# Kernel optimization log

Measured on AMD Instinct MI355X. Metric: run time of the kernel, lower is better.

The kernel has to match this reference:

```python
import jax, jax.numpy as jnp
import numpy as np

# Dimensions: B jets, P max particles, C coords, F features, K neighbors,
# H hidden units, O MLP output dim. Edge feature dim E = 2*(C+F).
B, P, C, F, K, H, O = 256, 128, 2, 7, 16, 128, 256
E = 2 * (C + F)
BIG = 1e9  # distance assigned to invalid (padded) neighbors


def setup_inputs() -> dict:
    key = jax.random.key(0)
    k1, k2, k3, k4 = jax.random.split(key, 4)
    raw = jax.random.normal(k1, (B, P, C + F), dtype=jnp.float32)
    # per-jet particle counts in [K+2, P]; padding is contiguous at the end
    lengths = jax.random.randint(k2, (B,), K + 2, P + 1)
    mask = (jnp.arange(P)[None, :] < lengths[:, None]).astype(jnp.float32)  # [B,P]
    # zero out padded rows and append mask as the last column (as the layer expects)
    x = jnp.concatenate([raw * mask[..., None], mask[..., None]], axis=-1)  # [B,P,C+F+1]
    W1 = jax.random.normal(k3, (E, H), dtype=jnp.float32) * (1.0 / np.sqrt(E))
    b1 = jnp.zeros((H,), dtype=jnp.float32)
    W2 = jax.random.normal(k4, (H, O), dtype=jnp.float32) * (1.0 / np.sqrt(H))
    b2 = jnp.zeros((O,), dtype=jnp.float32)
    return {"x": x, "W1": W1, "b1": b1, "W2": W2, "b2": b2}


def reference(x, W1, b1, W2, b2):
    coords = x[..., :C]          # [B,P,C]
    feats = x[..., C:-1]         # [B,P,F]
    mask = x[..., -1]            # [B,P] 1=real particle, 0=padding
    valid = mask > 0

    # --- kNN on coordinates (masked, vectorized over jets) ---
    diff = coords[:, :, None, :] - coords[:, None, :, :]      # [B,P,P,C]
    # squared distance: same ordering as tf.norm, avoids sqrt-at-zero issues
    dist2 = jnp.sum(diff * diff, axis=-1)                      # [B,P,P]
    dist2 = jnp.where(valid[:, None, :], dist2, BIG)           # mask padded neighbors
    _, idx = jax.lax.top_k(-dist2, K + 1)                      # [B,P,K+1]
    idx = idx[..., 1:]                                         # drop self -> [B,P,K]

    # --- gather neighbor coords/features ---
    idx_flat = idx.reshape(B, P * K)
    nbr_c = jnp.take_along_axis(coords, idx_flat[..., None], axis=1).reshape(B, P, K, C)
    nbr_f = jnp.take_along_axis(feats, idx_flat[..., None], axis=1).reshape(B, P, K, F)
    ctr_c = jnp.broadcast_to(coords[:, :, None, :], (B, P, K, C))
    ctr_f = jnp.broadcast_to(feats[:, :, None, :], (B, P, K, F))

    # edge features: [coord_i, feat_i, coord_j - coord_i, feat_j - feat_i]
    edge = jnp.concatenate([ctr_c, ctr_f, nbr_c - ctr_c, nbr_f - ctr_f], axis=-1)  # [B,P,K,E]

    # --- MLP + mean aggregation over neighbors ---
    h = jax.nn.relu(edge @ W1 + b1)   # [B,P,K,H]
    h = jax.nn.relu(h @ W2 + b2)      # [B,P,K,O]
    avg = jnp.mean(h, axis=2)         # [B,P,O]

    # append mask column; zero out padded particles (matches _fix_number_of_particles)
    out = jnp.concatenate([avg, jnp.ones((B, P, 1), avg.dtype)], axis=-1) * mask[..., None]
    return out
```

## Files before the change

kernel.cpp:

```cpp
#include <hip/hip_runtime.h>

#define BB 256
#define PP 128
#define KK 16
#define HH 128
#define OO 256
#define EE 18
#define XCH 10
#define BIGD 1000000000.0f
#define GPT 16
#define PH 8
#define NBLK ((BB * PP) / GPT)

typedef __bf16 bf16x8 __attribute__((ext_vector_type(8)));
typedef __bf16 bf16x4 __attribute__((ext_vector_type(4)));
typedef float  f32x4  __attribute__((ext_vector_type(4)));

__global__ __launch_bounds__(256) void pack_w_kernel(const float* __restrict__ W1,
                                                     const float* __restrict__ W2,
                                                     __bf16* __restrict__ W2p,
                                                     __bf16* __restrict__ W1p) {
    const int t = blockIdx.x * 256 + threadIdx.x;
    if (t < 32768) {
        const int j  = t & 7;
        const int l  = (t >> 3) & 63;
        const int ks = (t >> 9) & 3;
        const int ct = t >> 11;
        const int row = ks * 32 + ((l >> 4) * 8) + j;
        const int col = ct * 16 + (l & 15);
        W2p[t] = (__bf16)W2[row * OO + col];
    } else {
        const int t2 = t - 32768;
        const int j  = t2 & 7;
        const int l  = (t2 >> 3) & 63;
        const int nt = t2 >> 9;
        const int k  = ((l >> 4) * 8) + j;
        const int n  = nt * 16 + (l & 15);
        W1p[t2] = (k < EE) ? (__bf16)W1[k * HH + n] : (__bf16)0.0f;
    }
}

__global__ __launch_bounds__(256, 4) void mlp_kernel(const float* __restrict__ x,
                                                     const __bf16* __restrict__ W1p,
                                                     const float* __restrict__ b1,
                                                     const __bf16* __restrict__ W2p,
                                                     const float* __restrict__ b2,
                                                     float* __restrict__ out) {
    __shared__ __bf16 sh1A[4 * PH * 64 * 8];
    __shared__ int    sknn[PH][KK];

    const int tid = threadIdx.x;
    const int lane = tid & 63;
    const int w = tid >> 6;
    const int quad = lane >> 4;
    const int lcol = lane & 15;

    const int pbase = blockIdx.x * GPT;
    const int bidx = pbase >> 7;
    const int i0 = pbase & (PP - 1);
    const float* xb = x + (size_t)bidx * PP * XCH;
    float* outrow = out + (size_t)pbase * (OO + 1);

    bf16x8 wf[8];
#pragma unroll
    for (int nt = 0; nt < 8; ++nt)
        wf[nt] = *(const bf16x8*)&W1p[(size_t)((nt * 64 + lane) * 8)];

    const f32x4 z4 = {0.0f, 0.0f, 0.0f, 0.0f};

#pragma unroll
    for (int h = 0; h < 2; ++h) {
        const int r0 = h * PH;

        const float mph = xb[(i0 + r0 + (lane & 7)) * XCH + (XCH - 1)];
        if (__all(mph == 0.0f)) {
            for (int o = tid; o < PH * (OO + 1); o += 256)
                outrow[(size_t)r0 * (OO + 1) + o] = 0.0f;
            continue;
        }

        const int j0 = lane, j1 = lane + 64;
        const float2 c0 = *(const float2*)(xb + j0 * XCH);
        const float  m0 = xb[j0 * XCH + (XCH - 1)];
        const float2 c1 = *(const float2*)(xb + j1 * XCH);
        const float  m1 = xb[j1 * XCH + (XCH - 1)];

#pragma unroll 1
        for (int p = 0; p < 2; ++p) {
            const int g = w * 2 + p;
            const int ip = i0 + r0 + g;
            const float2 cc = *(const float2*)(xb + ip * XCH);
            const float mwp = xb[ip * XCH + (XCH - 1)];
            if (mwp != 0.0f) {
                float d0, d1;
                {
                    float dx = cc.x - c0.x, dy = cc.y - c0.y;
                    d0 = __fadd_rn(__fmul_rn(dx, dx), __fmul_rn(dy, dy));
                    if (m0 <= 0.0f || j0 == ip) d0 = BIGD;
                }
                {
                    float dx = cc.x - c1.x, dy = cc.y - c1.y;
                    d1 = __fadd_rn(__fmul_rn(dx, dx), __fmul_rn(dy, dy));
                    if (m1 <= 0.0f || j1 == ip) d1 = BIGD;
                }

                const unsigned d0b = __float_as_uint(d0);
                const unsigned d1b = __float_as_uint(d1);

                unsigned long long A0 = ~0ull, A1 = ~0ull, W0 = 0ull, W1 = 0ull;
                int need = KK;
                int asz = 2 * 64;

                auto step = [&](unsigned long long q0, unsigned long long q1) {
                    const unsigned long long z0 = A0 & q0;
                    const unsigned long long z1 = A1 & q1;
                    const int c = __popcll(z0) + __popcll(z1);
                    if (c == need) { W0 |= z0; W1 |= z1; A0 = A1 = 0ull; need = 0; }
                    else if (c > need) { A0 = z0; A1 = z1; asz = c; }
                    else { W0 |= z0; W1 |= z1; need -= c; A0 &= ~z0; A1 &= ~z1; asz -= c; }
                };

#pragma unroll 1
                for (int t = 14; t >= 0; --t) {
                    const unsigned dg0 = (d0b >> (2 * t + 1)) & 3u;
                    const unsigned dg1 = (d1b >> (2 * t + 1)) & 3u;
                    const unsigned long long p0_0  = __ballot(dg0 == 0u);
                    const unsigned long long p1_0  = __ballot(dg1 == 0u);
                    const unsigned long long p0_01 = __ballot(dg0 <= 1u);
                    const unsigned long long p1_01 = __ballot(dg1 <= 1u);
                    const unsigned long long p0_02 = __ballot(dg0 <= 2u);
                    const unsigned long long p1_02 = __ballot(dg1 <= 2u);
                    const unsigned long long z0_0  = A0 & p0_0,  z1_0  = A1 & p1_0;
                    const unsigned long long z0_01 = A0 & p0_01, z1_01 = A1 & p1_01;
                    const unsigned long long z0_02 = A0 & p0_02, z1_02 = A1 & p1_02;
                    const int c0c  = __popcll(z0_0)  + __popcll(z1_0);
                    const int c01 = __popcll(z0_01) + __popcll(z1_01);
                    const int c02 = __popcll(z0_02) + __popcll(z1_02);
                    if (c0c >= need) {
                        A0 = z0_0; A1 = z1_0; asz = c0c;
                    } else if (c01 >= need) {
                        W0 |= z0_0; W1 |= z1_0; need -= c0c;
                        A0 = z0_01 & ~p0_0; A1 = z1_01 & ~p1_0; asz = c01 - c0c;
                    } else if (c02 >= need) {
                        W0 |= z0_01; W1 |= z1_01; need -= c01;
                        A0 = z0_02 & ~p0_01; A1 = z1_02 & ~p1_01; asz = c02 - c01;
                    } else {
                        W0 |= z0_02; W1 |= z1_02; need -= c02;
                        A0 &= ~p0_02; A1 &= ~p1_02; asz -= c02;
                    }
                    if (asz == need) { W0 |= A0; W1 |= A1; A0 = A1 = 0ull; need = 0; break; }
                }
                if (need) {
                    const unsigned long long q0 = __ballot((d0b & 1u) == 0u);
                    const unsigned long long q1 = __ballot((d1b & 1u) == 0u);
                    step(q0, q1);
                }
                if (need) step(~0ull, 0ull);
                {
                    const unsigned long long M5 = 0x00000000FFFFFFFFull;
                    const unsigned long long M4 = 0x0000FFFF0000FFFFull;
                    const unsigned long long M3 = 0x00FF00FF00FF00FFull;
                    const unsigned long long M2 = 0x0F0F0F0F0F0F0F0Full;
                    const unsigned long long M1 = 0x3333333333333333ull;
                    const unsigned long long M0 = 0x5555555555555555ull;
                    if (need) step(M5, M5);
                    if (need) step(M4, M4);
                    if (need) step(M3, M3);
                    if (need) step(M2, M2);
                    if (need) step(M1, M1);
                    if (need) step(M0, M0);
                }
                W0 |= A0; W1 |= A1;

                unsigned int mb0 = __builtin_amdgcn_mbcnt_lo((unsigned)(W0 & 0xffffffffull), 0u);
                mb0 = __builtin_amdgcn_mbcnt_hi((unsigned)(W0 >> 32), mb0);
                unsigned int mb1 = __builtin_amdgcn_mbcnt_lo((unsigned)(W1 & 0xffffffffull), 0u);
                mb1 = __builtin_amdgcn_mbcnt_hi((unsigned)(W1 >> 32), mb1);
                const int base1 = __popcll(W0);

                if ((W0 >> lane) & 1ull) sknn[g][mb0] = j0;
                if ((W1 >> lane) & 1ull) sknn[g][base1 + mb1] = j1;
            } else {
                if (lane < KK) sknn[g][lane] = 0;
            }
        }

#pragma unroll
        for (int p = 0; p < 2; ++p) {
            const int g = w * 2 + p;
            const int ip = i0 + r0 + g;
            const int jn = sknn[g][lcol];
            const float* ciP = xb + ip * XCH;
            const float* cjP = xb + jn * XCH;
            const float2 a01 = *(const float2*)(ciP + 0);
            const float2 a23 = *(const float2*)(ciP + 2);
            const float2 a45 = *(const float2*)(ciP + 4);
            const float2 a67 = *(const float2*)(ciP + 6);
            const float  a8  = ciP[8];
            const float2 n01 = *(const float2*)(cjP + 0);
            const float2 n23 = *(const float2*)(cjP + 2);
            const float2 n45 = *(const float2*)(cjP + 4);
            const float2 n67 = *(const float2*)(cjP + 6);
            const float  n8  = cjP[8];

            float v[8];
#pragma unroll
            for (int e = 0; e < 8; ++e) v[e] = 0.0f;
            if (quad == 0) {
                v[0] = a01.x; v[1] = a01.y; v[2] = a23.x; v[3] = a23.y;
                v[4] = a45.x; v[5] = a45.y; v[6] = a67.x; v[7] = a67.y;
            } else if (quad == 1) {
                v[0] = a8;
                v[1] = n01.x - a01.x; v[2] = n01.y - a01.y;
                v[3] = n23.x - a23.x; v[4] = n23.y - a23.y;
                v[5] = n45.x - a45.x; v[6] = n45.y - a45.y;
                v[7] = n67.x - a67.x;
            } else if (quad == 2) {
                v[0] = n67.y - a67.y;
                v[1] = n8 - a8;
            }

            bf16x8 ef;
#pragma unroll
            for (int e = 0; e < 8; ++e) ef[e] = (__bf16)v[e];

            f32x4 hh[8];
#pragma unroll
            for (int nt = 0; nt < 8; ++nt)
                hh[nt] = __builtin_amdgcn_mfma_f32_16x16x32_bf16(wf[nt], ef, z4, 0, 0, 0);

#pragma unroll
            for (int nt = 0; nt < 8; ++nt) {
                const int ks = nt >> 1;
                const int lp = (((nt * 2 + (quad >> 1)) & 3) << 4) | lcol;
                const f32x4 b1v = *(const f32x4*)&b1[nt * 16 + quad * 4];
                bf16x4 hv;
#pragma unroll
                for (int r = 0; r < 4; ++r)
                    hv[r] = (__bf16)fmaxf(hh[nt][r] + b1v[r], 0.0f);
                *(bf16x4*)&sh1A[((ks * PH + g) * 64 + lp) * 8 + (quad & 1) * 4] = hv;
            }
        }
        __syncthreads();

#pragma unroll
        for (int gg = 0; gg < 2; ++gg) {
#pragma unroll
            for (int ch = 0; ch < 2; ++ch) {
                f32x4 acc[4][2];
#pragma unroll
                for (int gi = 0; gi < 4; ++gi) { acc[gi][0] = z4; acc[gi][1] = z4; }

#pragma unroll
                for (int ks = 0; ks < 4; ++ks) {
                    bf16x8 af[4], bfr[2];
#pragma unroll
                    for (int gi = 0; gi < 4; ++gi)
                        af[gi] = *(const bf16x8*)&sh1A[((ks * PH + gg * 4 + gi) * 64 + lane) * 8];
#pragma unroll
                    for (int c = 0; c < 2; ++c)
                        bfr[c] = *(const bf16x8*)&W2p[(size_t)((((w * 4 + ch * 2 + c) * 4 + ks) * 64 + lane) * 8)];
#pragma unroll
                    for (int gi = 0; gi < 4; ++gi)
#pragma unroll
                        for (int c = 0; c < 2; ++c)
                            acc[gi][c] = __builtin_amdgcn_mfma_f32_16x16x32_bf16(
                                af[gi], bfr[c], acc[gi][c], 0, 0, 0);
                }

#pragma unroll
                for (int c = 0; c < 2; ++c) {
                    const int col = w * 64 + (ch * 2 + c) * 16 + lcol;
                    const float bc = b2[col];
                    float val = 0.0f;
#pragma unroll
                    for (int gi = 0; gi < 4; ++gi) {
                        float s = 0.0f;
#pragma unroll
                        for (int r = 0; r < 4; ++r) s += fmaxf(acc[gi][c][r] + bc, 0.0f);
                        s += __shfl_xor(s, 16, 64);
                        s += __shfl_xor(s, 32, 64);
                        if (quad == gi) val = s;
                    }
                    const float mp = xb[(i0 + r0 + gg * 4 + quad) * XCH + (XCH - 1)];
                    outrow[(size_t)(r0 + gg * 4 + quad) * (OO + 1) + col] = val * (mp * (1.0f / KK));
                }
            }
        }
        if (tid < PH)
            outrow[(size_t)(r0 + tid) * (OO + 1) + OO] = xb[(i0 + r0 + tid) * XCH + (XCH - 1)];

        __syncthreads();
    }
}

extern "C" void kernel_launch(void* const* d_in, const int* in_sizes, int n_in,
                              void* d_out, int out_size, void* d_ws, size_t ws_size,
                              hipStream_t stream) {
    const float* x  = (const float*)d_in[0];
    const float* W1 = (const float*)d_in[1];
    const float* b1 = (const float*)d_in[2];
    const float* W2 = (const float*)d_in[3];
    const float* b2 = (const float*)d_in[4];
    float* out = (float*)d_out;

    __bf16* W2p = (__bf16*)d_ws;
    __bf16* W1p = (__bf16*)((char*)d_ws + 65536);

    pack_w_kernel<<<144, 256, 0, stream>>>(W1, W2, W2p, W1p);

    mlp_kernel<<<NBLK, 256, 0, stream>>>(x, W1p, b1, W2p, b2, out);
}
```

Measured before the change: 133.1 us.

## Halve particles per block and interleave two radix-select kNN searches per wave

Each block now handles 8 particles instead of two sequential halves of 8, which doubles the grid and removes the inner half-loop and its extra barrier. Within each wave, the two particles' radix-select kNN loops are interleaved in one loop over digits, so their ballots and popcounts can overlap instead of running back to back. This adds latency hiding and more blocks for the scheduler. The cost is W1 fragment loads and x staging repeated per smaller block, plus extra registers for the two selection states.

```diff
diff --git a/kernel.cpp b/kernel.cpp
--- a/kernel.cpp
+++ b/kernel.cpp
@@ -8,13 +8,13 @@
 #define EE 18
 #define XCH 10
 #define BIGD 1000000000.0f
-#define GPT 16
-#define PH 8
+#define GPT 8
 #define NBLK ((BB * PP) / GPT)
 
 typedef __bf16 bf16x8 __attribute__((ext_vector_type(8)));
 typedef __bf16 bf16x4 __attribute__((ext_vector_type(4)));
 typedef float  f32x4  __attribute__((ext_vector_type(4)));
+typedef unsigned long long ull;
 
 __global__ __launch_bounds__(256) void pack_w_kernel(const float* __restrict__ W1,
                                                      const float* __restrict__ W2,
@@ -46,8 +46,8 @@
                                                      const __bf16* __restrict__ W2p,
                                                      const float* __restrict__ b2,
                                                      float* __restrict__ out) {
-    __shared__ __bf16 sh1A[4 * PH * 64 * 8];
-    __shared__ int    sknn[PH][KK];
+    __shared__ __bf16 sh1A[4 * GPT * 64 * 8];
+    __shared__ int    sknn[GPT][KK];
 
     const int tid = threadIdx.x;
     const int lane = tid & 63;
@@ -61,237 +61,251 @@
     const float* xb = x + (size_t)bidx * PP * XCH;
     float* outrow = out + (size_t)pbase * (OO + 1);
 
+    const float mph = xb[(i0 + (lane & 7)) * XCH + (XCH - 1)];
+    if (__all(mph == 0.0f)) {
+        for (int o = tid; o < GPT * (OO + 1); o += 256) outrow[o] = 0.0f;
+        return;
+    }
+
+    const int j0 = lane, j1 = lane + 64;
+    const float2 c0 = *(const float2*)(xb + j0 * XCH);
+    const float  m0 = xb[j0 * XCH + (XCH - 1)];
+    const float2 c1 = *(const float2*)(xb + j1 * XCH);
+    const float  m1 = xb[j1 * XCH + (XCH - 1)];
+
+    const int gA = w * 2, gB = w * 2 + 1;
+    const int iA = i0 + gA, iB = i0 + gB;
+    const float2 ccA = *(const float2*)(xb + iA * XCH);
+    const float  mA  = xb[iA * XCH + (XCH - 1)];
+    const float2 ccB = *(const float2*)(xb + iB * XCH);
+    const float  mB  = xb[iB * XCH + (XCH - 1)];
+
     bf16x8 wf[8];
 #pragma unroll
     for (int nt = 0; nt < 8; ++nt)
         wf[nt] = *(const bf16x8*)&W1p[(size_t)((nt * 64 + lane) * 8)];
 
-    const f32x4 z4 = {0.0f, 0.0f, 0.0f, 0.0f};
-
-#pragma unroll
-    for (int h = 0; h < 2; ++h) {
-        const int r0 = h * PH;
-
-        const float mph = xb[(i0 + r0 + (lane & 7)) * XCH + (XCH - 1)];
-        if (__all(mph == 0.0f)) {
-            for (int o = tid; o < PH * (OO + 1); o += 256)
-                outrow[(size_t)r0 * (OO + 1) + o] = 0.0f;
-            continue;
-        }
-
-        const int j0 = lane, j1 = lane + 64;
-        const float2 c0 = *(const float2*)(xb + j0 * XCH);
-        const float  m0 = xb[j0 * XCH + (XCH - 1)];
-        const float2 c1 = *(const float2*)(xb + j1 * XCH);
-        const float  m1 = xb[j1 * XCH + (XCH - 1)];
+    unsigned db0[2], db1[2];
+    {
+        float dx, dy, d;
+        dx = ccA.x - c0.x; dy = ccA.y - c0.y;
+        d = __fadd_rn(__fmul_rn(dx, dx), __fmul_rn(dy, dy));
+        if (m0 <= 0.0f || j0 == iA) d = BIGD;
+        db0[0] = __float_as_uint(d);
+        dx = ccA.x - c1.x; dy = ccA.y - c1.y;
+        d = __fadd_rn(__fmul_rn(dx, dx), __fmul_rn(dy, dy));
+        if (m1 <= 0.0f || j1 == iA) d = BIGD;
+        db1[0] = __float_as_uint(d);
+        dx = ccB.x - c0.x; dy = ccB.y - c0.y;
+        d = __fadd_rn(__fmul_rn(dx, dx), __fmul_rn(dy, dy));
+        if (m0 <= 0.0f || j0 == iB) d = BIGD;
+        db0[1] = __float_as_uint(d);
+        dx = ccB.x - c1.x; dy = ccB.y - c1.y;
+        d = __fadd_rn(__fmul_rn(dx, dx), __fmul_rn(dy, dy));
+        if (m1 <= 0.0f || j1 == iB) d = BIGD;
+        db1[1] = __float_as_uint(d);
+    }
+
+    const bool act[2] = {mA != 0.0f, mB != 0.0f};
+    ull A0[2], A1[2], W0[2], W1g[2];
+    int need[2], asz[2];
+#pragma unroll
+    for (int p = 0; p < 2; ++p) {
+        A0[p] = ~0ull; A1[p] = ~0ull; W0[p] = 0ull; W1g[p] = 0ull;
+        need[p] = act[p] ? KK : 0;
+        asz[p] = 128;
+    }
 
 #pragma unroll 1
+    for (int t = 14; t >= 0; --t) {
+#pragma unroll
         for (int p = 0; p < 2; ++p) {
-            const int g = w * 2 + p;
-            const int ip = i0 + r0 + g;
-            const float2 cc = *(const float2*)(xb + ip * XCH);
-            const float mwp = xb[ip * XCH + (XCH - 1)];
-            if (mwp != 0.0f) {
-                float d0, d1;
-                {
-                    float dx = cc.x - c0.x, dy = cc.y - c0.y;
-                    d0 = __fadd_rn(__fmul_rn(dx, dx), __fmul_rn(dy, dy));
-                    if (m0 <= 0.0f || j0 == ip) d0 = BIGD;
+            if (need[p]) {
+                const unsigned dg0 = (db0[p] >> (2 * t + 1)) & 3u;
+                const unsigned dg1 = (db1[p] >> (2 * t + 1)) & 3u;
+                const ull p0_0  = __ballot(dg0 == 0u);
+                const ull p1_0  = __ballot(dg1 == 0u);
+                const ull p0_01 = __ballot(dg0 <= 1u);
+                const ull p1_01 = __ballot(dg1 <= 1u);
+                const ull p0_02 = __ballot(dg0 <= 2u);
+                const ull p1_02 = __ballot(dg1 <= 2u);
+                const ull z0_0  = A0[p] & p0_0,  z1_0  = A1[p] & p1_0;
+                const ull z0_01 = A0[p] & p0_01, z1_01 = A1[p] & p1_01;
+                const ull z0_02 = A0[p] & p0_02, z1_02 = A1[p] & p1_02;
+                const int c0c = __popcll(z0_0)  + __popcll(z1_0);
+                const int c01 = __popcll(z0_01) + __popcll(z1_01);
+                const int c02 = __popcll(z0_02) + __popcll(z1_02);
+                if (c0c >= need[p]) {
+                    A0[p] = z0_0; A1[p] = z1_0; asz[p] = c0c;
+                } else if (c01 >= need[p]) {
+                    W0[p] |= z0_0; W1g[p] |= z1_0; need[p] -= c0c;
+                    A0[p] = z0_01 & ~p0_0; A1[p] = z1_01 & ~p1_0; asz[p] = c01 - c0c;
+                } else if (c02 >= need[p]) {
+                    W0[p] |= z0_01; W1g[p] |= z1_01; need[p] -= c01;
+                    A0[p] = z0_02 & ~p0_01; A1[p] = z1_02 & ~p1_01; asz[p] = c02 - c01;
+                } else {
+                    W0[p] |= z0_02; W1g[p] |= z1_02; need[p] -= c02;
+                    A0[p] &= ~p0_02; A1[p] &= ~p1_02; asz[p] -= c02;
                 }
-                {
-                    float dx = cc.x - c1.x, dy = cc.y - c1.y;
-                    d1 = __fadd_rn(__fmul_rn(dx, dx), __fmul_rn(dy, dy));
-                    if (m1 <= 0.0f || j1 == ip) d1 = BIGD;
-                }
-
-                const unsigned d0b = __float_as_uint(d0);
-                const unsigned d1b = __float_as_uint(d1);
-
-                unsigned long long A0 = ~0ull, A1 = ~0ull, W0 = 0ull, W1 = 0ull;
-                int need = KK;
-                int asz = 2 * 64;
-
-                auto step = [&](unsigned long long q0, unsigned long long q1) {
-                    const unsigned long long z0 = A0 & q0;
-                    const unsigned long long z1 = A1 & q1;
-                    const int c = __popcll(z0) + __popcll(z1);
-                    if (c == need) { W0 |= z0; W1 |= z1; A0 = A1 = 0ull; need = 0; }
-                    else if (c > need) { A0 = z0; A1 = z1; asz = c; }
-                    else { W0 |= z0; W1 |= z1; need -= c; A0 &= ~z0; A1 &= ~z1; asz -= c; }
-                };
-
-#pragma unroll 1
-                for (int t = 14; t >= 0; --t) {
-                    const unsigned dg0 = (d0b >> (2 * t + 1)) & 3u;
-                    const unsigned dg1 = (d1b >> (2 * t + 1)) & 3u;
-                    const unsigned long long p0_0  = __ballot(dg0 == 0u);
-                    const unsigned long long p1_0  = __ballot(dg1 == 0u);
-                    const unsigned long long p0_01 = __ballot(dg0 <= 1u);
-                    const unsigned long long p1_01 = __ballot(dg1 <= 1u);
-                    const unsigned long long p0_02 = __ballot(dg0 <= 2u);
-                    const unsigned long long p1_02 = __ballot(dg1 <= 2u);
-                    const unsigned long long z0_0  = A0 & p0_0,  z1_0  = A1 & p1_0;
-                    const unsigned long long z0_01 = A0 & p0_01, z1_01 = A1 & p1_01;
-                    const unsigned long long z0_02 = A0 & p0_02, z1_02 = A1 & p1_02;
-                    const int c0c  = __popcll(z0_0)  + __popcll(z1_0);
-                    const int c01 = __popcll(z0_01) + __popcll(z1_01);
-                    const int c02 = __popcll(z0_02) + __popcll(z1_02);
-                    if (c0c >= need) {
-                        A0 = z0_0; A1 = z1_0; asz = c0c;
-                    } else if (c01 >= need) {
-                        W0 |= z0_0; W1 |= z1_0; need -= c0c;
-                        A0 = z0_01 & ~p0_0; A1 = z1_01 & ~p1_0; asz = c01 - c0c;
-                    } else if (c02 >= need) {
-                        W0 |= z0_01; W1 |= z1_01; need -= c01;
-                        A0 = z0_02 & ~p0_01; A1 = z1_02 & ~p1_01; asz = c02 - c01;
-                    } else {
-                        W0 |= z0_02; W1 |= z1_02; need -= c02;
-                        A0 &= ~p0_02; A1 &= ~p1_02; asz -= c02;
-                    }
-                    if (asz == need) { W0 |= A0; W1 |= A1; A0 = A1 = 0ull; need = 0; break; }
-                }
-                if (need) {
-                    const unsigned long long q0 = __ballot((d0b & 1u) == 0u);
-                    const unsigned long long q1 = __ballot((d1b & 1u) == 0u);
-                    step(q0, q1);
-                }
-                if (need) step(~0ull, 0ull);
-                {
-                    const unsigned long long M5 = 0x00000000FFFFFFFFull;
-                    const unsigned long long M4 = 0x0000FFFF0000FFFFull;
-                    const unsigned long long M3 = 0x00FF00FF00FF00FFull;
-                    const unsigned long long M2 = 0x0F0F0F0F0F0F0F0Full;
-                    const unsigned long long M1 = 0x3333333333333333ull;
-                    const unsigned long long M0 = 0x5555555555555555ull;
-                    if (need) step(M5, M5);
-                    if (need) step(M4, M4);
-                    if (need) step(M3, M3);
-                    if (need) step(M2, M2);
-                    if (need) step(M1, M1);
-                    if (need) step(M0, M0);
-                }
-                W0 |= A0; W1 |= A1;
-
-                unsigned int mb0 = __builtin_amdgcn_mbcnt_lo((unsigned)(W0 & 0xffffffffull), 0u);
-                mb0 = __builtin_amdgcn_mbcnt_hi((unsigned)(W0 >> 32), mb0);
-                unsigned int mb1 = __builtin_amdgcn_mbcnt_lo((unsigned)(W1 & 0xffffffffull), 0u);
-                mb1 = __builtin_amdgcn_mbcnt_hi((unsigned)(W1 >> 32), mb1);
-                const int base1 = __popcll(W0);
-
-                if ((W0 >> lane) & 1ull) sknn[g][mb0] = j0;
-                if ((W1 >> lane) & 1ull) sknn[g][base1 + mb1] = j1;
-            } else {
-                if (lane < KK) sknn[g][lane] = 0;
-            }
-        }
-
-#pragma unroll
-        for (int p = 0; p < 2; ++p) {
-            const int g = w * 2 + p;
-            const int ip = i0 + r0 + g;
-            const int jn = sknn[g][lcol];
-            const float* ciP = xb + ip * XCH;
-            const float* cjP = xb + jn * XCH;
-            const float2 a01 = *(const float2*)(ciP + 0);
-            const float2 a23 = *(const float2*)(ciP + 2);
-            const float2 a45 = *(const float2*)(ciP + 4);
-            const float2 a67 = *(const float2*)(ciP + 6);
-            const float  a8  = ciP[8];
-            const float2 n01 = *(const float2*)(cjP + 0);
-            const float2 n23 = *(const float2*)(cjP + 2);
-            const float2 n45 = *(const float2*)(cjP + 4);
-            const float2 n67 = *(const float2*)(cjP + 6);
-            const float  n8  = cjP[8];
-
-            float v[8];
-#pragma unroll
-            for (int e = 0; e < 8; ++e) v[e] = 0.0f;
-            if (quad == 0) {
-                v[0] = a01.x; v[1] = a01.y; v[2] = a23.x; v[3] = a23.y;
-                v[4] = a45.x; v[5] = a45.y; v[6] = a67.x; v[7] = a67.y;
-            } else if (quad == 1) {
-                v[0] = a8;
-                v[1] = n01.x - a01.x; v[2] = n01.y - a01.y;
-                v[3] = n23.x - a23.x; v[4] = n23.y - a23.y;
-                v[5] = n45.x - a45.x; v[6] = n45.y - a45.y;
-                v[7] = n67.x - a67.x;
-            } else if (quad == 2) {
-                v[0] = n67.y - a67.y;
-                v[1] = n8 - a8;
-            }
-
-            bf16x8 ef;
-#pragma unroll
-            for (int e = 0; e < 8; ++e) ef[e] = (__bf16)v[e];
-
-            f32x4 hh[8];
-#pragma unroll
-            for (int nt = 0; nt < 8; ++nt)
-                hh[nt] = __builtin_amdgcn_mfma_f32_16x16x32_bf16(wf[nt], ef, z4, 0, 0, 0);
-
-#pragma unroll
-            for (int nt = 0; nt < 8; ++nt) {
-                const int ks = nt >> 1;
-                const int lp = (((nt * 2 + (quad >> 1)) & 3) << 4) | lcol;
-                const f32x4 b1v = *(const f32x4*)&b1[nt * 16 + quad * 4];
-                bf16x4 hv;
-#pragma unroll
-                for (int r = 0; r < 4; ++r)
-                    hv[r] = (__bf16)fmaxf(hh[nt][r] + b1v[r], 0.0f);
-                *(bf16x4*)&sh1A[((ks * PH + g) * 64 + lp) * 8 + (quad & 1) * 4] = hv;
-            }
-        }
-        __syncthreads();
-
-#pragma unroll
-        for (int gg = 0; gg < 2; ++gg) {
-#pragma unroll
-            for (int ch = 0; ch < 2; ++ch) {
-                f32x4 acc[4][2];
-#pragma unroll
-                for (int gi = 0; gi < 4; ++gi) { acc[gi][0] = z4; acc[gi][1] = z4; }
-
-#pragma unroll
-                for (int ks = 0; ks < 4; ++ks) {
-                    bf16x8 af[4], bfr[2];
-#pragma unroll
-                    for (int gi = 0; gi < 4; ++gi)
-                        af[gi] = *(const bf16x8*)&sh1A[((ks * PH + gg * 4 + gi) * 64 + lane) * 8];
-#pragma unroll
-                    for (int c = 0; c < 2; ++c)
-                        bfr[c] = *(const bf16x8*)&W2p[(size_t)((((w * 4 + ch * 2 + c) * 4 + ks) * 64 + lane) * 8)];
-#pragma unroll
-                    for (int gi = 0; gi < 4; ++gi)
-#pragma unroll
-                        for (int c = 0; c < 2; ++c)
-                            acc[gi][c] = __builtin_amdgcn_mfma_f32_16x16x32_bf16(
-                                af[gi], bfr[c], acc[gi][c], 0, 0, 0);
-                }
-
-#pragma unroll
-                for (int c = 0; c < 2; ++c) {
-                    const int col = w * 64 + (ch * 2 + c) * 16 + lcol;
-                    const float bc = b2[col];
-                    float val = 0.0f;
-#pragma unroll
-                    for (int gi = 0; gi < 4; ++gi) {
-                        float s = 0.0f;
-#pragma unroll
-                        for (int r = 0; r < 4; ++r) s += fmaxf(acc[gi][c][r] + bc, 0.0f);
-                        s += __shfl_xor(s, 16, 64);
-                        s += __shfl_xor(s, 32, 64);
-                        if (quad == gi) val = s;
-                    }
-                    const float mp = xb[(i0 + r0 + gg * 4 + quad) * XCH + (XCH - 1)];
-                    outrow[(size_t)(r0 + gg * 4 + quad) * (OO + 1) + col] = val * (mp * (1.0f / KK));
+                if (asz[p] == need[p]) {
+                    W0[p] |= A0[p]; W1g[p] |= A1[p];
+                    A0[p] = A1[p] = 0ull; need[p] = 0;
                 }
             }
         }
-        if (tid < PH)
-            outrow[(size_t)(r0 + tid) * (OO + 1) + OO] = xb[(i0 + r0 + tid) * XCH + (XCH - 1)];
-
-        __syncthreads();
-    }
+        if (!(need[0] | need[1])) break;
+    }
+#pragma unroll
+    for (int p = 0; p < 2; ++p) {
+        auto stepP = [&](ull q0, ull q1) {
+            const ull z0 = A0[p] & q0;
+            const ull z1 = A1[p] & q1;
+            const int c = __popcll(z0) + __popcll(z1);
+            if (c == need[p]) { W0[p] |= z0; W1g[p] |= z1; A0[p] = A1[p] = 0ull; need[p] = 0; }
+            else if (c > need[p]) { A0[p] = z0; A1[p] = z1; asz[p] = c; }
+            else { W0[p] |= z0; W1g[p] |= z1; need[p] -= c; A0[p] &= ~z0; A1[p] &= ~z1; asz[p] -= c; }
+        };
+        if (need[p]) {
+            const ull q0 = __ballot((db0[p] & 1u) == 0u);
+            const ull q1 = __ballot((db1[p] & 1u) == 0u);
+            stepP(q0, q1);
+        }
+        if (need[p]) stepP(~0ull, 0ull);
+        {
+            const ull M5 = 0x00000000FFFFFFFFull;
+            const ull M4 = 0x0000FFFF0000FFFFull;
+            const ull M3 = 0x00FF00FF00FF00FFull;
+            const ull M2 = 0x0F0F0F0F0F0F0F0Full;
+            const ull M1 = 0x3333333333333333ull;
+            const ull M0 = 0x5555555555555555ull;
+            if (need[p]) stepP(M5, M5);
+            if (need[p]) stepP(M4, M4);
+            if (need[p]) stepP(M3, M3);
+            if (need[p]) stepP(M2, M2);
+            if (need[p]) stepP(M1, M1);
+            if (need[p]) stepP(M0, M0);
+        }
+        W0[p] |= A0[p]; W1g[p] |= A1[p];
+
+        const int g = w * 2 + p;
+        if (act[p]) {
+            unsigned int mb0 = __builtin_amdgcn_mbcnt_lo((unsigned)(W0[p] & 0xffffffffull), 0u);
+            mb0 = __builtin_amdgcn_mbcnt_hi((unsigned)(W0[p] >> 32), mb0);
+            unsigned int mb1 = __builtin_amdgcn_mbcnt_lo((unsigned)(W1g[p] & 0xffffffffull), 0u);
+            mb1 = __builtin_amdgcn_mbcnt_hi((unsigned)(W1g[p] >> 32), mb1);
+            const int base1 = __popcll(W0[p]);
+            if ((W0[p] >> lane) & 1ull) sknn[g][mb0] = j0;
+            if ((W1g[p] >> lane) & 1ull) sknn[g][base1 + mb1] = j1;
+        } else {
+            if (lane < KK) sknn[g][lane] = 0;
+        }
+    }
+
+    const f32x4 z4 = {0.0f, 0.0f, 0.0f, 0.0f};
+#pragma unroll
+    for (int p = 0; p < 2; ++p) {
+        const int g = w * 2 + p;
+        const int ip = i0 + g;
+        const int jn = sknn[g][lcol];
+        const float* ciP = xb + ip * XCH;
+        const float* cjP = xb + jn * XCH;
+        const float2 a01 = *(const float2*)(ciP + 0);
+        const float2 a23 = *(const float2*)(ciP + 2);
+        const float2 a45 = *(const float2*)(ciP + 4);
+        const float2 a67 = *(const float2*)(ciP + 6);
+        const float  a8  = ciP[8];
+        const float2 n01 = *(const float2*)(cjP + 0);
+        const float2 n23 = *(const float2*)(cjP + 2);
+        const float2 n45 = *(const float2*)(cjP + 4);
+        const float2 n67 = *(const float2*)(cjP + 6);
+        const float  n8  = cjP[8];
+
+        float v[8];
+#pragma unroll
+        for (int e = 0; e < 8; ++e) v[e] = 0.0f;
+        if (quad == 0) {
+            v[0] = a01.x; v[1] = a01.y; v[2] = a23.x; v[3] = a23.y;
+            v[4] = a45.x; v[5] = a45.y; v[6] = a67.x; v[7] = a67.y;
+        } else if (quad == 1) {
+            v[0] = a8;
+            v[1] = n01.x - a01.x; v[2] = n01.y - a01.y;
+            v[3] = n23.x - a23.x; v[4] = n23.y - a23.y;
+            v[5] = n45.x - a45.x; v[6] = n45.y - a45.y;
+            v[7] = n67.x - a67.x;
+        } else if (quad == 2) {
+            v[0] = n67.y - a67.y;
+            v[1] = n8 - a8;
+        }
+
+        bf16x8 ef;
+#pragma unroll
+        for (int e = 0; e < 8; ++e) ef[e] = (__bf16)v[e];
+
+        f32x4 hh[8];
+#pragma unroll
+        for (int nt = 0; nt < 8; ++nt)
+            hh[nt] = __builtin_amdgcn_mfma_f32_16x16x32_bf16(wf[nt], ef, z4, 0, 0, 0);
+
+#pragma unroll
+        for (int nt = 0; nt < 8; ++nt) {
+            const int ks = nt >> 1;
+            const int lp = (((nt * 2 + (quad >> 1)) & 3) << 4) | lcol;
+            const f32x4 b1v = *(const f32x4*)&b1[nt * 16 + quad * 4];
+            bf16x4 hv;
+#pragma unroll
+            for (int r = 0; r < 4; ++r)
+                hv[r] = (__bf16)fmaxf(hh[nt][r] + b1v[r], 0.0f);
+            *(bf16x4*)&sh1A[((ks * GPT + g) * 64 + lp) * 8 + (quad & 1) * 4] = hv;
+        }
+    }
+    __syncthreads();
+
+#pragma unroll
+    for (int gg = 0; gg < 2; ++gg) {
+#pragma unroll
+        for (int ch = 0; ch < 2; ++ch) {
+            f32x4 acc[4][2];
+#pragma unroll
+            for (int gi = 0; gi < 4; ++gi) { acc[gi][0] = z4; acc[gi][1] = z4; }
+
+#pragma unroll
+            for (int ks = 0; ks < 4; ++ks) {
+                bf16x8 af[4], bfr[2];
+#pragma unroll
+                for (int gi = 0; gi < 4; ++gi)
+                    af[gi] = *(const bf16x8*)&sh1A[((ks * GPT + gg * 4 + gi) * 64 + lane) * 8];
+#pragma unroll
+                for (int c = 0; c < 2; ++c)
+                    bfr[c] = *(const bf16x8*)&W2p[(size_t)((((w * 4 + ch * 2 + c) * 4 + ks) * 64 + lane) * 8)];
+#pragma unroll
+                for (int gi = 0; gi < 4; ++gi)
+#pragma unroll
+                    for (int c = 0; c < 2; ++c)
+                        acc[gi][c] = __builtin_amdgcn_mfma_f32_16x16x32_bf16(
+                            af[gi], bfr[c], acc[gi][c], 0, 0, 0);
+            }
+
+#pragma unroll
+            for (int c = 0; c < 2; ++c) {
+                const int col = w * 64 + (ch * 2 + c) * 16 + lcol;
+                const float bc = b2[col];
+                float val = 0.0f;
+#pragma unroll
+                for (int gi = 0; gi < 4; ++gi) {
+                    float s = 0.0f;
+#pragma unroll
+                    for (int r = 0; r < 4; ++r) s += fmaxf(acc[gi][c][r] + bc, 0.0f);
+                    s += __shfl_xor(s, 16, 64);
+                    s += __shfl_xor(s, 32, 64);
+                    if (quad == gi) val = s;
+                }
+                const float mp = xb[(i0 + gg * 4 + quad) * XCH + (XCH - 1)];
+                outrow[(size_t)(gg * 4 + quad) * (OO + 1) + col] = val * (mp * (1.0f / KK));
+            }
+        }
+    }
+    if (tid < GPT)
+        outrow[(size_t)tid * (OO + 1) + OO] = xb[(i0 + tid) * XCH + (XCH - 1)];
 }
 
 extern "C" void kernel_launch(void* const* d_in, const int* in_sizes, int n_in,
```

After: 126.6 us. 4.9% less time.
